# Optimization experiments

Hardware: AMD Instinct MI355X
Metric: run time of the kernel (lower is better)

Reference implementation:

```python
import jax, jax.numpy as jnp
from jax import lax
import numpy as np

KERNEL = 3
PAD = KERNEL // 2


def _normalized_weights(affinity):
    # affinity: [B, 8, H, W] -> 9-tap weights [B, 9, H, W] with center at index 4
    aff_sum = jnp.sum(jnp.abs(affinity), axis=1, keepdims=True)
    aff_norm = affinity / aff_sum
    center = 1.0 - jnp.sum(aff_norm, axis=1, keepdims=True)
    # Original loop uses affinity channels 0..3 for taps before center, 4..7 after
    return jnp.concatenate([aff_norm[:, :4], center, aff_norm[:, 4:]], axis=1)


def setup_inputs() -> dict:
    key = jax.random.key(0)
    k1, k2 = jax.random.split(key)
    B, H, W = 8, 480, 640
    affinity = jax.random.normal(k1, (B, KERNEL * KERNEL - 1, H, W), dtype=jnp.float32)
    feature = jax.random.normal(k2, (B, 1, H, W), dtype=jnp.float32)
    return {"affinity": affinity, "feature": feature, "times": 24}


def reference(affinity, feature, times):
    weights = _normalized_weights(affinity)  # [B, 9, H, W]
    B, C, H, W = feature.shape

    def step(f, _):
        fp = jnp.pad(f, ((0, 0), (0, 0), (PAD, PAD), (PAD, PAD)))
        # 9 shifted views stacked on a tap axis: [B, 9, C, H, W]
        shifts = jnp.stack(
            [fp[:, :, i:i + H, j:j + W] for i in range(KERNEL) for j in range(KERNEL)],
            axis=1,
        )
        f_new = jnp.sum(shifts * weights[:, :, None, :, :], axis=1)
        return f_new, None

    out, _ = lax.scan(step, feature, None, length=times)
    return out
```

## Files before the change

kernel.cpp:

```cpp
#include <hip/hip_runtime.h>
#include <hip/hip_fp16.h>
#include <cstddef>


#define HIMG 480
#define WIMG 640
#define HW   (HIMG * WIMG)
#define BN   8

#define TILE   40
#define TSTEPS 12
#define IH     13
#define WHL    12
#define SW     (TILE + 2 * IH)
#define PITCH  68
#define NT     512
#define UXN    16
#define UYN    32

#define WS_FRAME_B  ((size_t)BN * HW * 4)
#define WS_WA_B     ((size_t)BN * HW * 16)
#define WS_WC_B     ((size_t)BN * HW * 4)
#define WS_NEED     (WS_FRAME_B + WS_WA_B + WS_WC_B)

__global__ __launch_bounds__(256) void precompute_w(
    const float* __restrict__ aff,
    __half2* __restrict__ wA,
    float* __restrict__ wC)
{
    int i = blockIdx.x * 256 + threadIdx.x;
    int b = i / HW;
    int p = i - b * HW;
    const float* a = aff + (size_t)b * 8 * HW + p;

    float w[8];
    float s = 0.f;
    #pragma unroll
    for (int c = 0; c < 8; ++c) { w[c] = a[(size_t)c * HW]; s += fabsf(w[c]); }
    float r = 1.0f / s;
    float acc = 0.f;
    #pragma unroll
    for (int c = 0; c < 8; ++c) { w[c] *= r; acc += w[c]; }
    float ctr = 1.0f - acc;

    union { float4 f4; __half2 h[4]; } u;
    u.h[0] = __floats2half2_rn(w[0], w[1]);
    u.h[1] = __floats2half2_rn(w[2], w[3]);
    u.h[2] = __floats2half2_rn(w[4], w[5]);
    u.h[3] = __floats2half2_rn(w[6], w[7]);
    *(float4*)(wA + 4 * (size_t)i) = u.f4;
    wC[i] = ctr;
}

#define TAPS(P, ra, rb, rc, J)                                    \
  ( wcc[P] * rb[(J) + 1]                                          \
  + __low2float (wv[P][0]) * ra[(J)    ]                          \
  + __high2float(wv[P][0]) * ra[(J) + 1]                          \
  + __low2float (wv[P][1]) * ra[(J) + 2]                          \
  + __high2float(wv[P][1]) * rb[(J)    ]                          \
  + __low2float (wv[P][2]) * rb[(J) + 2]                          \
  + __high2float(wv[P][2]) * rc[(J)    ]                          \
  + __low2float (wv[P][3]) * rc[(J) + 1]                          \
  + __high2float(wv[P][3]) * rc[(J) + 2] )

#define LOAD6(r, p) do {                                          \
    float4 q_ = *(const float4*)(p);                              \
    float2 t_ = *(const float2*)((p) + 4);                        \
    r[0] = q_.x; r[1] = q_.y; r[2] = q_.z; r[3] = q_.w;           \
    r[4] = t_.x; r[5] = t_.y; } while (0)

template <bool PRE>
__global__ __launch_bounds__(NT, 4) void affprop12(
    const float* __restrict__ aff,
    const __half2* __restrict__ wA,
    const float* __restrict__ wC,
    const float* __restrict__ src,
    float* __restrict__ dst)
{
    __shared__ __align__(16) float fA[SW * PITCH];
    __shared__ __align__(16) float fB[SW * PITCH];

    const int tid = threadIdx.x;
    const int ox  = blockIdx.x * TILE;
    const int oy  = blockIdx.y * TILE;
    const int b   = blockIdx.z;

    const float* __restrict__ sb = src + (size_t)b * HW;
    float*       __restrict__ db = dst + (size_t)b * HW;

    for (int i = tid; i < SW * SW; i += NT) {
        int r  = i / SW;
        int c  = i - r * SW;
        int gy = oy - IH + r;
        int gx = ox - IH + c;
        float v = 0.f;
        if ((unsigned)gy < (unsigned)HIMG && (unsigned)gx < (unsigned)WIMG)
            v = sb[gy * WIMG + gx];
        fA[r * PITCH + c] = v;
    }
    for (int i = tid; i < SW * PITCH / 4; i += NT)
        *(float4*)&fB[4 * i] = make_float4(0.f, 0.f, 0.f, 0.f);

    const int ux = tid & (UXN - 1);
    const int uy = tid >> 4;

    __half2 wv[8][4];
    float   wcc[8];

    #pragma unroll
    for (int p = 0; p < 8; ++p) {
        int py = p >> 2, j = p & 3;
        int gy = oy - WHL + 2 * uy + py;
        int gx = ox - WHL + 4 * ux + j;
        bool in = (unsigned)gy < (unsigned)HIMG && (unsigned)gx < (unsigned)WIMG;
        if (PRE) {
            if (in) {
                size_t idx = (size_t)b * HW + (size_t)gy * WIMG + gx;
                union { float4 f4; __half2 h[4]; } u;
                u.f4 = *(const float4*)(wA + 4 * idx);
                wv[p][0] = u.h[0]; wv[p][1] = u.h[1];
                wv[p][2] = u.h[2]; wv[p][3] = u.h[3];
                wcc[p] = wC[idx];
            } else {
                __half2 z = __floats2half2_rn(0.f, 0.f);
                wv[p][0] = z; wv[p][1] = z; wv[p][2] = z; wv[p][3] = z;
                wcc[p] = 0.f;
            }
        } else {
            float w[8];
            float s = 0.f;
            if (in) {
                const float* ap = aff + (size_t)b * 8 * HW + (size_t)gy * WIMG + gx;
                #pragma unroll
                for (int c = 0; c < 8; ++c) { w[c] = ap[(size_t)c * HW]; s += fabsf(w[c]); }
            } else {
                #pragma unroll
                for (int c = 0; c < 8; ++c) w[c] = 0.f;
                s = 1.f;
            }
            float rr  = in ? 1.0f / s : 0.f;
            float acc = 0.f;
            #pragma unroll
            for (int c = 0; c < 8; ++c) { w[c] *= rr; acc += w[c]; }
            wv[p][0] = __floats2half2_rn(w[0], w[1]);
            wv[p][1] = __floats2half2_rn(w[2], w[3]);
            wv[p][2] = __floats2half2_rn(w[4], w[5]);
            wv[p][3] = __floats2half2_rn(w[6], w[7]);
            wcc[p] = in ? 1.0f - acc : 0.f;
        }
    }
    __syncthreads();

    const float* fin = fA;
    float*       fo  = fB;
    const int rbase = 2 * uy;
    const int cbase = 4 * ux;

    #pragma unroll 1
    for (int s = 0; s < TSTEPS; ++s) {
        const float* rp = fin + rbase * PITCH + cbase;
        float r0[6], r1[6], r2[6], r3[6];
        LOAD6(r0, rp);
        LOAD6(r1, rp + PITCH);
        LOAD6(r2, rp + 2 * PITCH);
        LOAD6(r3, rp + 3 * PITCH);

        float* wp0 = fo + (rbase + 1) * PITCH + cbase + 1;
        {
            float a0 = TAPS(0, r0, r1, r2, 0);
            float a1 = TAPS(1, r0, r1, r2, 1);
            float a2 = TAPS(2, r0, r1, r2, 2);
            float a3 = TAPS(3, r0, r1, r2, 3);
            wp0[0] = a0;
            *(float2*)(wp0 + 1) = make_float2(a1, a2);
            wp0[3] = a3;
        }
        {
            float a0 = TAPS(4, r1, r2, r3, 0);
            float a1 = TAPS(5, r1, r2, r3, 1);
            float a2 = TAPS(6, r1, r2, r3, 2);
            float a3 = TAPS(7, r1, r2, r3, 3);
            float* wp1 = wp0 + PITCH;
            wp1[0] = a0;
            *(float2*)(wp1 + 1) = make_float2(a1, a2);
            wp1[3] = a3;
        }
        __syncthreads();
        const float* t = fin; fin = fo; fo = (float*)t;
    }

    if (tid < TILE * (TILE / 4) / 1) {
    }
    {
        int i = tid;
        if (i < TILE * (TILE / 4)) {
            int r  = i / (TILE / 4);
            int c4 = (i - r * (TILE / 4)) * 4;
            const float* p = fin + (IH + r) * PITCH + IH + c4;
            float4 v = make_float4(p[0], p[1], p[2], p[3]);
            *(float4*)&db[(size_t)(oy + r) * WIMG + ox + c4] = v;
        }
    }
}

extern "C" void kernel_launch(void* const* d_in, const int* in_sizes, int n_in,
                              void* d_out, int out_size, void* d_ws, size_t ws_size,
                              hipStream_t stream)
{
    const float* aff  = (const float*)d_in[0];
    const float* feat = (const float*)d_in[1];
    float* out = (float*)d_out;

    char* ws = (char*)d_ws;
    float*   wsFrame = (float*)ws;
    __half2* wA      = (__half2*)(ws + WS_FRAME_B);
    float*   wC      = (float*)(ws + WS_FRAME_B + WS_WA_B);

    dim3 blk(NT, 1, 1);
    dim3 grd(WIMG / TILE, HIMG / TILE, BN);

    if (ws_size >= WS_NEED) {
        precompute_w<<<dim3(BN * HW / 256), dim3(256), 0, stream>>>(aff, wA, wC);
        affprop12<true><<<grd, blk, 0, stream>>>(aff, wA, wC, feat, wsFrame);
        affprop12<true><<<grd, blk, 0, stream>>>(aff, wA, wC, wsFrame, out);
    } else {
        affprop12<false><<<grd, blk, 0, stream>>>(aff, nullptr, nullptr, feat, wsFrame);
        affprop12<false><<<grd, blk, 0, stream>>>(aff, nullptr, nullptr, wsFrame, out);
    }
}
```

Before: 264.3 us.

## Fuse weight precompute into first propagation pass and remap threads to column strips

The separate weight-normalization kernel is removed. The first propagation launch now normalizes the affinities itself and writes the packed half-precision weights for its tile interior to the workspace, and the second launch reuses them. The per-thread work mapping changes from 2x4 output patches to one column of 8 rows with a sliding 3-row register window. This makes shared-memory and global weight accesses consecutive across lanes, at the cost of more scalar LDS loads. The first pass now re-reads raw affinity over the whole haloed tile, which is redundant work in exchange for one fewer launch and one fewer full weight round trip.

```diff
diff --git a/kernel.cpp b/kernel.cpp
--- a/kernel.cpp
+++ b/kernel.cpp
@@ -12,73 +12,25 @@
 #define TSTEPS 12
 #define IH     13
 #define WHL    12
-#define SW     (TILE + 2 * IH)
+#define SW     66
 #define PITCH  68
 #define NT     512
-#define UXN    16
-#define UYN    32
 
 #define WS_FRAME_B  ((size_t)BN * HW * 4)
 #define WS_WA_B     ((size_t)BN * HW * 16)
 #define WS_WC_B     ((size_t)BN * HW * 4)
 #define WS_NEED     (WS_FRAME_B + WS_WA_B + WS_WC_B)
 
-__global__ __launch_bounds__(256) void precompute_w(
+template <int MODE>
+__global__ __launch_bounds__(NT, 4) void affprop12(
     const float* __restrict__ aff,
     __half2* __restrict__ wA,
-    float* __restrict__ wC)
-{
-    int i = blockIdx.x * 256 + threadIdx.x;
-    int b = i / HW;
-    int p = i - b * HW;
-    const float* a = aff + (size_t)b * 8 * HW + p;
-
-    float w[8];
-    float s = 0.f;
-    #pragma unroll
-    for (int c = 0; c < 8; ++c) { w[c] = a[(size_t)c * HW]; s += fabsf(w[c]); }
-    float r = 1.0f / s;
-    float acc = 0.f;
-    #pragma unroll
-    for (int c = 0; c < 8; ++c) { w[c] *= r; acc += w[c]; }
-    float ctr = 1.0f - acc;
-
-    union { float4 f4; __half2 h[4]; } u;
-    u.h[0] = __floats2half2_rn(w[0], w[1]);
-    u.h[1] = __floats2half2_rn(w[2], w[3]);
-    u.h[2] = __floats2half2_rn(w[4], w[5]);
-    u.h[3] = __floats2half2_rn(w[6], w[7]);
-    *(float4*)(wA + 4 * (size_t)i) = u.f4;
-    wC[i] = ctr;
-}
-
-#define TAPS(P, ra, rb, rc, J)                                    \
-  ( wcc[P] * rb[(J) + 1]                                          \
-  + __low2float (wv[P][0]) * ra[(J)    ]                          \
-  + __high2float(wv[P][0]) * ra[(J) + 1]                          \
-  + __low2float (wv[P][1]) * ra[(J) + 2]                          \
-  + __high2float(wv[P][1]) * rb[(J)    ]                          \
-  + __low2float (wv[P][2]) * rb[(J) + 2]                          \
-  + __high2float(wv[P][2]) * rc[(J)    ]                          \
-  + __low2float (wv[P][3]) * rc[(J) + 1]                          \
-  + __high2float(wv[P][3]) * rc[(J) + 2] )
-
-#define LOAD6(r, p) do {                                          \
-    float4 q_ = *(const float4*)(p);                              \
-    float2 t_ = *(const float2*)((p) + 4);                        \
-    r[0] = q_.x; r[1] = q_.y; r[2] = q_.z; r[3] = q_.w;           \
-    r[4] = t_.x; r[5] = t_.y; } while (0)
-
-template <bool PRE>
-__global__ __launch_bounds__(NT, 4) void affprop12(
-    const float* __restrict__ aff,
-    const __half2* __restrict__ wA,
-    const float* __restrict__ wC,
+    float* __restrict__ wC,
     const float* __restrict__ src,
     float* __restrict__ dst)
 {
-    __shared__ __align__(16) float fA[SW * PITCH];
-    __shared__ __align__(16) float fB[SW * PITCH];
+    __shared__ float fA[SW * PITCH];
+    __shared__ float fB[SW * PITCH];
 
     const int tid = threadIdx.x;
     const int ox  = blockIdx.x * TILE;
@@ -101,30 +53,31 @@
     for (int i = tid; i < SW * PITCH / 4; i += NT)
         *(float4*)&fB[4 * i] = make_float4(0.f, 0.f, 0.f, 0.f);
 
-    const int ux = tid & (UXN - 1);
-    const int uy = tid >> 4;
+    const int c  = tid & 63;
+    const int g  = tid >> 6;
+    const int sc = c + 1;
 
     __half2 wv[8][4];
     float   wcc[8];
 
     #pragma unroll
-    for (int p = 0; p < 8; ++p) {
-        int py = p >> 2, j = p & 3;
-        int gy = oy - WHL + 2 * uy + py;
-        int gx = ox - WHL + 4 * ux + j;
-        bool in = (unsigned)gy < (unsigned)HIMG && (unsigned)gx < (unsigned)WIMG;
-        if (PRE) {
+    for (int i = 0; i < 8; ++i) {
+        const int gy = oy - WHL + 8 * g + i;
+        const int gx = ox - WHL + c;
+        const bool in = (unsigned)gy < (unsigned)HIMG && (unsigned)gx < (unsigned)WIMG;
+        const size_t idx = (size_t)b * HW + (size_t)gy * WIMG + gx;
+
+        if (MODE == 1) {
             if (in) {
-                size_t idx = (size_t)b * HW + (size_t)gy * WIMG + gx;
                 union { float4 f4; __half2 h[4]; } u;
                 u.f4 = *(const float4*)(wA + 4 * idx);
-                wv[p][0] = u.h[0]; wv[p][1] = u.h[1];
-                wv[p][2] = u.h[2]; wv[p][3] = u.h[3];
-                wcc[p] = wC[idx];
+                wv[i][0] = u.h[0]; wv[i][1] = u.h[1];
+                wv[i][2] = u.h[2]; wv[i][3] = u.h[3];
+                wcc[i] = wC[idx];
             } else {
                 __half2 z = __floats2half2_rn(0.f, 0.f);
-                wv[p][0] = z; wv[p][1] = z; wv[p][2] = z; wv[p][3] = z;
-                wcc[p] = 0.f;
+                wv[i][0] = z; wv[i][1] = z; wv[i][2] = z; wv[i][3] = z;
+                wcc[i] = 0.f;
             }
         } else {
             float w[8];
@@ -132,74 +85,78 @@
             if (in) {
                 const float* ap = aff + (size_t)b * 8 * HW + (size_t)gy * WIMG + gx;
                 #pragma unroll
-                for (int c = 0; c < 8; ++c) { w[c] = ap[(size_t)c * HW]; s += fabsf(w[c]); }
+                for (int k = 0; k < 8; ++k) { w[k] = ap[(size_t)k * HW]; s += fabsf(w[k]); }
             } else {
                 #pragma unroll
-                for (int c = 0; c < 8; ++c) w[c] = 0.f;
+                for (int k = 0; k < 8; ++k) w[k] = 0.f;
                 s = 1.f;
             }
             float rr  = in ? 1.0f / s : 0.f;
             float acc = 0.f;
             #pragma unroll
-            for (int c = 0; c < 8; ++c) { w[c] *= rr; acc += w[c]; }
-            wv[p][0] = __floats2half2_rn(w[0], w[1]);
-            wv[p][1] = __floats2half2_rn(w[2], w[3]);
-            wv[p][2] = __floats2half2_rn(w[4], w[5]);
-            wv[p][3] = __floats2half2_rn(w[6], w[7]);
-            wcc[p] = in ? 1.0f - acc : 0.f;
+            for (int k = 0; k < 8; ++k) { w[k] *= rr; acc += w[k]; }
+
+            union { float4 f4; __half2 h[4]; } u;
+            u.h[0] = __floats2half2_rn(w[0], w[1]);
+            u.h[1] = __floats2half2_rn(w[2], w[3]);
+            u.h[2] = __floats2half2_rn(w[4], w[5]);
+            u.h[3] = __floats2half2_rn(w[6], w[7]);
+            wv[i][0] = u.h[0]; wv[i][1] = u.h[1];
+            wv[i][2] = u.h[2]; wv[i][3] = u.h[3];
+            wcc[i] = in ? 1.0f - acc : 0.f;
+
+            if (MODE == 0) {
+                if ((unsigned)(gy - oy) < (unsigned)TILE &&
+                    (unsigned)(gx - ox) < (unsigned)TILE) {
+                    *(float4*)(wA + 4 * idx) = u.f4;
+                    wC[idx] = wcc[i];
+                }
+            }
         }
     }
     __syncthreads();
 
     const float* fin = fA;
     float*       fo  = fB;
-    const int rbase = 2 * uy;
-    const int cbase = 4 * ux;
 
     #pragma unroll 1
     for (int s = 0; s < TSTEPS; ++s) {
-        const float* rp = fin + rbase * PITCH + cbase;
-        float r0[6], r1[6], r2[6], r3[6];
-        LOAD6(r0, rp);
-        LOAD6(r1, rp + PITCH);
-        LOAD6(r2, rp + 2 * PITCH);
-        LOAD6(r3, rp + 3 * PITCH);
+        const float* rp = fin + (8 * g) * PITCH + c;
+        float a0 = rp[0], a1 = rp[1], a2 = rp[2];
+        rp += PITCH;
+        float b0 = rp[0], b1 = rp[1], b2 = rp[2];
+        float* wp = fo + (8 * g + 1) * PITCH + sc;
 
-        float* wp0 = fo + (rbase + 1) * PITCH + cbase + 1;
-        {
-            float a0 = TAPS(0, r0, r1, r2, 0);
-            float a1 = TAPS(1, r0, r1, r2, 1);
-            float a2 = TAPS(2, r0, r1, r2, 2);
-            float a3 = TAPS(3, r0, r1, r2, 3);
-            wp0[0] = a0;
-            *(float2*)(wp0 + 1) = make_float2(a1, a2);
-            wp0[3] = a3;
-        }
-        {
-            float a0 = TAPS(4, r1, r2, r3, 0);
-            float a1 = TAPS(5, r1, r2, r3, 1);
-            float a2 = TAPS(6, r1, r2, r3, 2);
-            float a3 = TAPS(7, r1, r2, r3, 3);
-            float* wp1 = wp0 + PITCH;
-            wp1[0] = a0;
-            *(float2*)(wp1 + 1) = make_float2(a1, a2);
-            wp1[3] = a3;
+        #pragma unroll
+        for (int i = 0; i < 8; ++i) {
+            rp += PITCH;
+            float c0 = rp[0], c1 = rp[1], c2 = rp[2];
+
+            float o = wcc[i] * b1
+                + __low2float (wv[i][0]) * a0
+                + __high2float(wv[i][0]) * a1
+                + __low2float (wv[i][1]) * a2
+                + __high2float(wv[i][1]) * b0
+                + __low2float (wv[i][2]) * b2
+                + __high2float(wv[i][2]) * c0
+                + __low2float (wv[i][3]) * c1
+                + __high2float(wv[i][3]) * c2;
+
+            *wp = o;
+            wp += PITCH;
+            a0 = b0; a1 = b1; a2 = b2;
+            b0 = c0; b1 = c1; b2 = c2;
         }
         __syncthreads();
         const float* t = fin; fin = fo; fo = (float*)t;
     }
 
-    if (tid < TILE * (TILE / 4) / 1) {
-    }
-    {
-        int i = tid;
-        if (i < TILE * (TILE / 4)) {
-            int r  = i / (TILE / 4);
-            int c4 = (i - r * (TILE / 4)) * 4;
-            const float* p = fin + (IH + r) * PITCH + IH + c4;
-            float4 v = make_float4(p[0], p[1], p[2], p[3]);
-            *(float4*)&db[(size_t)(oy + r) * WIMG + ox + c4] = v;
-        }
+    for (int i = tid; i < TILE * (TILE / 4); i += NT) {
+        int r  = i / (TILE / 4);
+        int c4 = (i - r * (TILE / 4)) * 4;
+        const float* p = fin + (IH + r) * PITCH + IH + c4;
+        float4 v = make_float4(p[0], p[1], p[2], p[3]);
+        *(float4*)&db[(size_t)(oy + r) * WIMG + ox + c4] = v;
     }
 }
 
@@ -220,11 +177,10 @@
     dim3 grd(WIMG / TILE, HIMG / TILE, BN);
 
     if (ws_size >= WS_NEED) {
-        precompute_w<<<dim3(BN * HW / 256), dim3(256), 0, stream>>>(aff, wA, wC);
-        affprop12<true><<<grd, blk, 0, stream>>>(aff, wA, wC, feat, wsFrame);
-        affprop12<true><<<grd, blk, 0, stream>>>(aff, wA, wC, wsFrame, out);
+        affprop12<0><<<grd, blk, 0, stream>>>(aff, wA, wC, feat, wsFrame);
+        affprop12<1><<<grd, blk, 0, stream>>>(aff, wA, wC, wsFrame, out);
     } else {
-        affprop12<false><<<grd, blk, 0, stream>>>(aff, nullptr, nullptr, feat, wsFrame);
-        affprop12<false><<<grd, blk, 0, stream>>>(aff, nullptr, nullptr, wsFrame, out);
+        affprop12<2><<<grd, blk, 0, stream>>>(aff, nullptr, nullptr, feat, wsFrame);
+        affprop12<2><<<grd, blk, 0, stream>>>(aff, nullptr, nullptr, wsFrame, out);
     }
 }
```

After: 219.9 us. -16.8%, faster.
